# Kernel optimization log

Measured on AMD Instinct MI355X. Metric: run time of the kernel, lower is better.

## Reference

```python
import jax, jax.numpy as jnp
import numpy as np

# model dims
V, D, C, H, NL, E, EH = 32000, 256, 2, 8, 2, 8, 1024
B, S = 16, 512
DH = D // H
N = B * S


def _pos_encoding(length, d):
    pos = jnp.arange(length)[:, None].astype(jnp.float32)
    div = jnp.exp(jnp.arange(0, d, 2).astype(jnp.float32) * (-np.log(10000.0) / d))
    pe = jnp.zeros((length, d), dtype=jnp.float32)
    pe = pe.at[:, 0::2].set(jnp.sin(pos * div))
    pe = pe.at[:, 1::2].set(jnp.cos(pos * div))
    return pe


def _ln(x, g, b, eps=1e-5):
    mu = x.mean(-1, keepdims=True)
    var = ((x - mu) ** 2).mean(-1, keepdims=True)
    return (x - mu) / jnp.sqrt(var + eps) * g + b


def setup_inputs():
    key = jax.random.key(0)
    ks = jax.random.split(key, 12)
    n = lambda k, shape, s=0.02: (jax.random.normal(k, shape) * s).astype(jnp.float32)
    return dict(
        x=jax.random.randint(ks[0], (B, S), 0, V),
        emb=n(ks[1], (V, D), 0.1),
        in_proj_w=n(ks[2], (NL, 3 * D, D)),
        in_proj_b=jnp.zeros((NL, 3 * D), jnp.float32),
        out_proj_w=n(ks[3], (NL, D, D)),
        out_proj_b=jnp.zeros((NL, D), jnp.float32),
        ln1_g=jnp.ones((NL, D), jnp.float32), ln1_b=jnp.zeros((NL, D), jnp.float32),
        ln2_g=jnp.ones((NL, D), jnp.float32), ln2_b=jnp.zeros((NL, D), jnp.float32),
        gate_w=n(ks[4], (NL, E, D)), gate_b=jnp.zeros((NL, E), jnp.float32),
        w1=n(ks[5], (NL, E, EH, D)), b1=jnp.zeros((NL, E, EH), jnp.float32),
        w2=n(ks[6], (NL, E, D, EH)), b2=jnp.zeros((NL, E, D), jnp.float32),
        fc1_w=n(ks[7], (128, D), 0.1), fc1_b=jnp.zeros((128,), jnp.float32),
        fc2_w=n(ks[8], (C, 128), 0.1), fc2_b=jnp.zeros((C,), jnp.float32),
    )


def reference(x, emb, in_proj_w, in_proj_b, out_proj_w, out_proj_b,
              ln1_g, ln1_b, ln2_g, ln2_b, gate_w, gate_b,
              w1, b1, w2, b2, fc1_w, fc1_b, fc2_w, fc2_b):
    h = emb[x] * np.sqrt(float(D))                       # [B,S,D]
    h = h + _pos_encoding(S, D)[None]
    pad = h.sum(-1) == 0                                 # key padding mask [B,S]
    for l in range(NL):
        # --- multi-head self-attention ---
        qkv = h @ in_proj_w[l].T + in_proj_b[l]          # [B,S,3D]
        q, k, v = jnp.split(qkv, 3, axis=-1)
        q = q.reshape(B, S, H, DH).transpose(0, 2, 1, 3)
        k = k.reshape(B, S, H, DH).transpose(0, 2, 1, 3)
        v = v.reshape(B, S, H, DH).transpose(0, 2, 1, 3)
        sc = jnp.einsum('bhqd,bhkd->bhqk', q, k) / np.sqrt(float(DH))
        sc = jnp.where(pad[:, None, None, :], -1e9, sc)
        a = jax.nn.softmax(sc, axis=-1)
        ctx = jnp.einsum('bhqk,bhkd->bhqd', a, v).transpose(0, 2, 1, 3).reshape(B, S, D)
        attn_out = ctx @ out_proj_w[l].T + out_proj_b[l]
        h = _ln(h + attn_out, ln1_g[l], ln1_b[l])
        # --- top-1 MoE ---
        xf = h.reshape(N, D)
        gwt = jax.nn.softmax(xf @ gate_w[l].T + gate_b[l], axis=-1)  # [N,E]
        top_idx = jnp.argmax(gwt, axis=-1)                # [N]
        top_w = jnp.max(gwt, axis=-1)                     # [N]
        eh = jax.nn.relu(jnp.einsum('nd,ehd->enh', xf, w1[l]) + b1[l][:, None, :])
        ey = jnp.einsum('enh,edh->end', eh, w2[l]) + b2[l][:, None, :]  # [E,N,D]
        sel = ey[top_idx, jnp.arange(N)]                  # gather routed expert output [N,D]
        moe = (top_w[:, None] * sel).reshape(B, S, D)
        h = _ln(h + moe, ln2_g[l], ln2_b[l])
    m = (~pad)[..., None].astype(h.dtype)                 # [B,S,1]
    pooled = (h * m).sum(1) / jnp.clip(m.sum(1), 1.0)     # masked mean pool [B,D]
    z = jax.nn.relu(pooled @ fc1_w.T + fc1_b)
    return z @ fc2_w.T + fc2_b                            # [B,C]
```

## Files before the change

kernel.cpp:

```cpp
#include <hip/hip_runtime.h>
#include <math.h>

#define D_MODEL 256
#define NTOK    8192
#define SEQ     512
#define NB      16
#define NH      8
#define DHEAD   32
#define NE      8
#define EHID    1024
#define CSTRIDE 32

typedef __attribute__((ext_vector_type(8))) short short8;
typedef __attribute__((ext_vector_type(4))) float floatx4;
typedef unsigned short ushort_t;

__device__ __forceinline__ ushort_t bf16r(float f) {
    unsigned int u = __float_as_uint(f);
    u += 0x7fffu + ((u >> 16) & 1u);
    return (ushort_t)(u >> 16);
}
__device__ __forceinline__ float bf2f(ushort_t b) {
    return __uint_as_float(((unsigned)b) << 16);
}

#define GLD16(gsrc, ldst) \
    __builtin_amdgcn_global_load_lds( \
        (const __attribute__((address_space(1))) void*)(gsrc), \
        (__attribute__((address_space(3))) void*)(ldst), 16, 0, 0)

__global__ __launch_bounds__(256) void wconv_all(
    const float* __restrict__ in_proj_w, const float* __restrict__ out_proj_w,
    const float* __restrict__ w1, const float* __restrict__ w2,
    ushort_t* __restrict__ wball)
{
    const int g = blockIdx.x * 256 + threadIdx.x;
    const float* src; ushort_t* dst; int lo;
    if (g < 98304)        { src = in_proj_w;  dst = wball;           lo = g; }
    else if (g < 131072)  { src = out_proj_w; dst = wball + 393216;  lo = g - 98304; }
    else if (g < 1179648) { src = w1;         dst = wball + 524288;  lo = g - 131072; }
    else                  { src = w2;         dst = wball + 4718592; lo = g - 1179648; }
    float4 v = *(const float4*)(src + (size_t)lo * 4);
    ushort_t o[4] = { bf16r(v.x), bf16r(v.y), bf16r(v.z), bf16r(v.w) };
    *(uint2*)(dst + (size_t)lo * 4) = *(uint2*)o;
}

__global__ __launch_bounds__(256) void embed_kernel(
    const int* __restrict__ x, const float* __restrict__ emb,
    float* __restrict__ h, ushort_t* __restrict__ hb, int* __restrict__ pad)
{
    __shared__ float wred[4];
    const int n = blockIdx.x;
    const int d = threadIdx.x;
    const int wave = d >> 6;
    const int s = n & (SEQ - 1);
    const int tok = x[n];
    float v = emb[tok * D_MODEL + d] * 16.0f;
    const int j = d >> 1;
    const float c = -9.210340371976184f / 256.0f;
    const float div = expf((float)(2 * j) * c);
    const float ang = (float)s * div;
    v += (d & 1) ? cosf(ang) : sinf(ang);
    h[n * D_MODEL + d] = v;
    hb[n * D_MODEL + d] = bf16r(v);
    float sm = v;
    for (int o = 1; o < 64; o <<= 1) sm += __shfl_xor(sm, o);
    if ((d & 63) == 0) wred[wave] = sm;
    __syncthreads();
    if (d == 0) pad[n] = ((wred[0] + wred[1] + wred[2] + wred[3]) == 0.0f) ? 1 : 0;
}

#define GF_RELU    1
#define GF_OUTBF16 2
#define GF_GATHER  4
#define GF_SCATTER 8

__global__ __launch_bounds__(256) void gemm_gl64(
    const ushort_t* __restrict__ A, const ushort_t* __restrict__ Bw,
    const float* __restrict__ bias, void* __restrict__ Cout,
    int M, int N, int K,
    const int* __restrict__ counts,
    const int* __restrict__ perm, const float* __restrict__ topw,
    int flags)
{
    __shared__ ushort_t As[64 * 64];
    __shared__ ushort_t Bs[64 * 64];
    const int e = blockIdx.z;
    int cnt, off = 0;
    if (counts) {
        cnt = counts[e * CSTRIDE];
        if ((int)blockIdx.y * 64 >= cnt) return;
        for (int i = 0; i < e; i++) off += counts[i * CSTRIDE];
    } else { cnt = M; }
    const ushort_t* Bp = Bw + (size_t)e * N * K;
    const float* bp = bias + (size_t)e * N;
    const int m0 = blockIdx.y * 64, n0 = blockIdx.x * 64;
    const int tid = threadIdx.x;
    const int lane = tid & 63, wave = tid >> 6;
    const int r8 = lane >> 3;
    const int p  = lane & 7;
    const int kswz = ((p ^ r8) << 3);
    const int row0 = wave * 16;
    size_t asrc[2], bsrc[2];
#pragma unroll
    for (int c = 0; c < 2; c++) {
        const int gr = m0 + row0 + c * 8 + r8;
        const int grc = (gr < cnt) ? gr : m0;
        asrc[c] = (flags & GF_GATHER) ? (size_t)perm[off + grc] : (size_t)(off + grc);
        bsrc[c] = (size_t)(n0 + row0 + c * 8 + r8);
    }
    const int quad = lane >> 4, fr = lane & 15;
    const int wm = (wave & 1) * 32, wn = (wave >> 1) * 32;
    floatx4 acc[2][2];
#pragma unroll
    for (int i = 0; i < 2; i++)
#pragma unroll
        for (int jj = 0; jj < 2; jj++) acc[i][jj] = (floatx4){0.f, 0.f, 0.f, 0.f};

    for (int k0 = 0; k0 < K; k0 += 64) {
        __syncthreads();
#pragma unroll
        for (int c = 0; c < 2; c++) {
            GLD16(A + asrc[c] * K + k0 + kswz, &As[(row0 + c * 8) * 64]);
            GLD16(Bp + bsrc[c] * K + k0 + kswz, &Bs[(row0 + c * 8) * 64]);
        }
        __syncthreads();
#pragma unroll
        for (int ks = 0; ks < 2; ks++) {
            const int sw = (((ks * 4 + quad) ^ (fr & 7)) << 3);
            short8 fa0 = *(const short8*)&As[(wm + fr) * 64 + sw];
            short8 fa1 = *(const short8*)&As[(wm + 16 + fr) * 64 + sw];
            short8 fb0 = *(const short8*)&Bs[(wn + fr) * 64 + sw];
            short8 fb1 = *(const short8*)&Bs[(wn + 16 + fr) * 64 + sw];
            acc[0][0] = __builtin_amdgcn_mfma_f32_16x16x32_bf16(fa0, fb0, acc[0][0], 0, 0, 0);
            acc[0][1] = __builtin_amdgcn_mfma_f32_16x16x32_bf16(fa0, fb1, acc[0][1], 0, 0, 0);
            acc[1][0] = __builtin_amdgcn_mfma_f32_16x16x32_bf16(fa1, fb0, acc[1][0], 0, 0, 0);
            acc[1][1] = __builtin_amdgcn_mfma_f32_16x16x32_bf16(fa1, fb1, acc[1][1], 0, 0, 0);
        }
    }
    const int crow0 = quad * 4;
    const int ccol = fr;
#pragma unroll
    for (int m = 0; m < 2; m++) {
#pragma unroll
        for (int n = 0; n < 2; n++) {
            const int gcol = n0 + wn + n * 16 + ccol;
            const float bsv = bp[gcol];
#pragma unroll
            for (int r = 0; r < 4; r++) {
                const int grow = m0 + wm + m * 16 + crow0 + r;
                if (grow >= cnt) continue;
                float v = acc[m][n][r] + bsv;
                if (flags & GF_RELU) v = fmaxf(v, 0.f);
                if (flags & GF_SCATTER) {
                    const int tok = perm[off + grow];
                    ((float*)Cout)[(size_t)tok * N + gcol] = v * topw[tok];
                } else if (flags & GF_OUTBF16) {
                    ((ushort_t*)Cout)[(size_t)(off + grow) * N + gcol] = bf16r(v);
                } else {
                    ((float*)Cout)[(size_t)(off + grow) * N + gcol] = v;
                }
            }
        }
    }
}

__global__ __launch_bounds__(256) void attn_kernel(
    const ushort_t* __restrict__ qkvb, const int* __restrict__ pad,
    ushort_t* __restrict__ ctxb)
{
    __shared__ ushort_t Kt[64 * 40];
    __shared__ ushort_t Vt[32 * 72];
    __shared__ ushort_t Ps[64 * 72];
    __shared__ float padf[512];
    const int tid = threadIdx.x;
    const int lane = tid & 63;
    const int wave = tid >> 6;
    const int quad = lane >> 4;
    const int l16  = lane & 15;
    const int bid = blockIdx.x;
    const int qt = bid & 7;
    const int hh = (bid >> 3) & 7;
    const int b = bid >> 6;
    const int q0 = wave * 16;

    padf[tid]       = (float)pad[b * SEQ + tid];
    padf[tid + 256] = (float)pad[b * SEQ + 256 + tid];

    short8 qfrag = *(const short8*)(qkvb +
        (size_t)(b * SEQ + qt * 64 + q0 + l16) * 768 + hh * 32 + quad * 8);

    const int skey = tid >> 2;
    const int schunk = (tid & 3) * 8;

    floatx4 o0 = {0.f,0.f,0.f,0.f}, o1 = {0.f,0.f,0.f,0.f};
    float lsum[4] = {0.f, 0.f, 0.f, 0.f};
    const float scale = 0.17677669529663687f;

    for (int t = 0; t < 8; t++) {
        const int kbase = b * SEQ + t * 64;
        __syncthreads();
        uint4 kv = *(const uint4*)(qkvb + (size_t)(kbase + skey) * 768 + 256 + hh * 32 + schunk);
        *(uint4*)&Kt[skey * 40 + schunk] = kv;
        uint4 vv = *(const uint4*)(qkvb + (size_t)(kbase + skey) * 768 + 512 + hh * 32 + schunk);
        ushort_t vs[8]; *(uint4*)vs = vv;
#pragma unroll
        for (int j = 0; j < 8; j++) {
            const int d = schunk + j;
            Vt[d * 72 + (skey ^ ((d >> 3) << 3))] = vs[j];
        }
        __syncthreads();
        floatx4 sfr[4];
#pragma unroll
        for (int fn = 0; fn < 4; fn++) {
            short8 kf = *(const short8*)&Kt[(fn * 16 + l16) * 40 + quad * 8];
            sfr[fn] = __builtin_amdgcn_mfma_f32_16x16x32_bf16(
                qfrag, kf, (floatx4){0.f,0.f,0.f,0.f}, 0, 0, 0);
        }
#pragma unroll
        for (int fn = 0; fn < 4; fn++) {
            const int keyl = fn * 16 + l16;
            const float pv = padf[t * 64 + keyl];
#pragma unroll
            for (int r = 0; r < 4; r++) {
                float p = (pv != 0.f) ? 0.f : __expf(sfr[fn][r] * scale);
                ushort_t pb = bf16r(p);
                lsum[r] += bf2f(pb);
                Ps[(q0 + quad * 4 + r) * 72 + keyl] = pb;
            }
        }
#pragma unroll
        for (int kc = 0; kc < 2; kc++) {
            short8 pf = *(const short8*)&Ps[(q0 + l16) * 72 + kc * 32 + quad * 8];
            {
                const int d = l16;
                short8 vf = *(const short8*)&Vt[d * 72 + ((kc * 32 + quad * 8) ^ ((d >> 3) << 3))];
                o0 = __builtin_amdgcn_mfma_f32_16x16x32_bf16(pf, vf, o0, 0, 0, 0);
            }
            {
                const int d = 16 + l16;
                short8 vf = *(const short8*)&Vt[d * 72 + ((kc * 32 + quad * 8) ^ ((d >> 3) << 3))];
                o1 = __builtin_amdgcn_mfma_f32_16x16x32_bf16(pf, vf, o1, 0, 0, 0);
            }
        }
    }
#pragma unroll
    for (int r = 0; r < 4; r++) {
        float v = lsum[r];
        v += __shfl_xor(v, 1); v += __shfl_xor(v, 2);
        v += __shfl_xor(v, 4); v += __shfl_xor(v, 8);
        lsum[r] = 1.f / v;
    }
    const int nq = b * SEQ + qt * 64 + q0 + quad * 4;
#pragma unroll
    for (int r = 0; r < 4; r++) {
        ushort_t* outp = ctxb + (size_t)(nq + r) * 256 + hh * 32;
        outp[l16]      = bf16r(o0[r] * lsum[r]);
        outp[16 + l16] = bf16r(o1[r] * lsum[r]);
    }
}

template<bool GATE>
__global__ __launch_bounds__(256) void add_ln_t(
    float* __restrict__ h, const float* __restrict__ add,
    const float* __restrict__ g, const float* __restrict__ b,
    ushort_t* __restrict__ hb,
    const float* __restrict__ gw, const float* __restrict__ gb,
    int* __restrict__ top_idx, float* __restrict__ top_w)
{
    __shared__ float wred[8];
    __shared__ float ered[NE][4];
    const int n = blockIdx.x;
    const int d = threadIdx.x;
    const int wave = d >> 6;
    const float v = h[n * D_MODEL + d] + add[n * D_MODEL + d];
    float s = v;
    for (int o = 1; o < 64; o <<= 1) s += __shfl_xor(s, o);
    if ((d & 63) == 0) wred[wave] = s;
    __syncthreads();
    const float mu = (wred[0] + wred[1] + wred[2] + wred[3]) * (1.0f / 256.0f);
    const float c = v - mu;
    float cs = c * c;
    for (int o = 1; o < 64; o <<= 1) cs += __shfl_xor(cs, o);
    if ((d & 63) == 0) wred[4 + wave] = cs;
    __syncthreads();
    const float var = (wred[4] + wred[5] + wred[6] + wred[7]) * (1.0f / 256.0f);
    const float o = c * rsqrtf(var + 1e-5f) * g[d] + b[d];
    h[n * D_MODEL + d] = o;
    hb[n * D_MODEL + d] = bf16r(o);
    if (GATE) {
#pragma unroll
        for (int e = 0; e < NE; e++) {
            float pe = o * gw[e * D_MODEL + d];
            for (int of = 1; of < 64; of <<= 1) pe += __shfl_xor(pe, of);
            if ((d & 63) == 0) ered[e][wave] = pe;
        }
        __syncthreads();
        if (d == 0) {
            float best = -1e30f; int bi = 0;
            float lg[NE];
#pragma unroll
            for (int e = 0; e < NE; e++) {
                lg[e] = ered[e][0] + ered[e][1] + ered[e][2] + ered[e][3] + gb[e];
                if (lg[e] > best) { best = lg[e]; bi = e; }
            }
            float ssum = 0.0f;
#pragma unroll
            for (int e = 0; e < NE; e++) ssum += __expf(lg[e] - best);
            top_idx[n] = bi;
            top_w[n] = 1.0f / ssum;
        }
    }
}

__global__ __launch_bounds__(256) void bucket_kernel(
    const int* __restrict__ top_idx, int* __restrict__ pos,
    int* __restrict__ counts)
{
    __shared__ int hist[NE];
    __shared__ int base[NE];
    __shared__ int lpos[256];
    const int n = blockIdx.x * 256 + threadIdx.x;
    if (threadIdx.x < NE) hist[threadIdx.x] = 0;
    __syncthreads();
    const int e = top_idx[n];
    lpos[threadIdx.x] = atomicAdd(&hist[e], 1);
    __syncthreads();
    if (threadIdx.x < NE)
        base[threadIdx.x] = atomicAdd(&counts[threadIdx.x * CSTRIDE], hist[threadIdx.x]);
    __syncthreads();
    pos[n] = base[e] + lpos[threadIdx.x];
}

__global__ __launch_bounds__(256) void scatter_perm(
    const int* __restrict__ top_idx, const int* __restrict__ pos,
    const int* __restrict__ counts, int* __restrict__ perm)
{
    __shared__ int offs_s[NE];
    if (threadIdx.x < NE) {
        int a = 0;
        for (int i = 0; i < (int)threadIdx.x; i++) a += counts[i * CSTRIDE];
        offs_s[threadIdx.x] = a;
    }
    __syncthreads();
    const int n = blockIdx.x * 256 + threadIdx.x;
    if (n < NTOK) perm[offs_s[top_idx[n]] + pos[n]] = n;
}

__global__ __launch_bounds__(256) void pool1(
    const float* __restrict__ h, const int* __restrict__ pad,
    float* __restrict__ pooled, float* __restrict__ cntb)
{
    const int b = blockIdx.x, c = blockIdx.y, d = threadIdx.x;
    float s = 0.0f; int cnt = 0;
    for (int i = 0; i < 32; i++) {
        const int idx = b * SEQ + c * 32 + i;
        if (!pad[idx]) { s += h[(size_t)idx * D_MODEL + d]; cnt++; }
    }
    atomicAdd(&pooled[b * D_MODEL + d], s);
    if (d == 0) atomicAdd(&cntb[b], (float)cnt);
}

__global__ __launch_bounds__(128) void cls_kernel(
    const float* __restrict__ pooled, const float* __restrict__ cntb,
    const float* __restrict__ fc1w, const float* __restrict__ fc1b,
    const float* __restrict__ fc2w, const float* __restrict__ fc2b,
    float* __restrict__ out)
{
    __shared__ float zs[128];
    const int b = blockIdx.x;
    const int j = threadIdx.x;
    const float invc = 1.0f / fmaxf(cntb[b], 1.0f);
    float s = 0.0f;
    for (int d = 0; d < D_MODEL; d++) s += pooled[b * D_MODEL + d] * fc1w[j * D_MODEL + d];
    zs[j] = fmaxf(s * invc + fc1b[j], 0.0f);
    __syncthreads();
    if (j < 2) {
        float o = fc2b[j];
        for (int i = 0; i < 128; i++) o += zs[i] * fc2w[j * 128 + i];
        out[b * 2 + j] = o;
    }
}

extern "C" void kernel_launch(void* const* d_in, const int* in_sizes, int n_in,
                              void* d_out, int out_size, void* d_ws, size_t ws_size,
                              hipStream_t stream)
{
    const int*   x          = (const int*)d_in[0];
    const float* emb        = (const float*)d_in[1];
    const float* in_proj_w  = (const float*)d_in[2];
    const float* in_proj_b  = (const float*)d_in[3];
    const float* out_proj_w = (const float*)d_in[4];
    const float* out_proj_b = (const float*)d_in[5];
    const float* ln1_g      = (const float*)d_in[6];
    const float* ln1_b      = (const float*)d_in[7];
    const float* ln2_g      = (const float*)d_in[8];
    const float* ln2_b      = (const float*)d_in[9];
    const float* gate_w     = (const float*)d_in[10];
    const float* gate_b     = (const float*)d_in[11];
    const float* w1         = (const float*)d_in[12];
    const float* b1         = (const float*)d_in[13];
    const float* w2         = (const float*)d_in[14];
    const float* b2         = (const float*)d_in[15];
    const float* fc1_w      = (const float*)d_in[16];
    const float* fc1_b      = (const float*)d_in[17];
    const float* fc2_w      = (const float*)d_in[18];
    const float* fc2_b      = (const float*)d_in[19];
    float* out = (float*)d_out;

    float* ws = (float*)d_ws;
    float*    h      = ws;
    float*    tmp    = ws + 2097152;
    ushort_t* qkvb   = (ushort_t*)(ws + 4194304);
    ushort_t* ctxb   = (ushort_t*)(ws + 7340032);
    ushort_t* ehb    = (ushort_t*)(ws + 4194304);
    ushort_t* hb     = (ushort_t*)(ws + 8388608);
    float*    top_w  = ws + 9437184;
    float*    pooled = ws + 9445376;
    float*    cntb   = ws + 9449472;
    int*      counts = (int*)(ws + 9449488);
    int* ipart   = (int*)(ws + 9450000);
    int* pad     = ipart;
    int* top_idx = ipart + 8192;
    int* pos     = ipart + 16384;
    int* perm    = ipart + 24576;
    ushort_t* wball = (ushort_t*)(ws + 9482768);

    wconv_all<<<8704, 256, 0, stream>>>(in_proj_w, out_proj_w, w1, w2, wball);
    embed_kernel<<<NTOK, 256, 0, stream>>>(x, emb, h, hb, pad);
    hipMemsetAsync(pooled, 0, (4096 + 16 + 2 * NE * CSTRIDE) * sizeof(float), stream);

    for (int l = 0; l < 2; l++) {
        const ushort_t* inb_l  = wball + (size_t)l * 196608;
        const ushort_t* outb_l = wball + 393216 + (size_t)l * 65536;
        const ushort_t* w1b_l  = wball + 524288 + (size_t)l * 2097152;
        const ushort_t* w2b_l  = wball + 4718592 + (size_t)l * 2097152;
        int* counts_l = counts + l * NE * CSTRIDE;

        gemm_gl64<<<dim3(768 / 64, NTOK / 64, 1), 256, 0, stream>>>(
            hb, inb_l, in_proj_b + l * 768, qkvb, NTOK, 768, 256,
            nullptr, nullptr, nullptr, GF_OUTBF16);
        attn_kernel<<<NB * NH * (SEQ / 64), 256, 0, stream>>>(qkvb, pad, ctxb);
        gemm_gl64<<<dim3(256 / 64, NTOK / 64, 1), 256, 0, stream>>>(
            ctxb, outb_l, out_proj_b + l * 256, tmp, NTOK, 256, 256,
            nullptr, nullptr, nullptr, 0);
        add_ln_t<true><<<NTOK, 256, 0, stream>>>(
            h, tmp, ln1_g + l * 256, ln1_b + l * 256, hb,
            gate_w + l * NE * 256, gate_b + l * NE, top_idx, top_w);
        bucket_kernel<<<NTOK / 256, 256, 0, stream>>>(top_idx, pos, counts_l);
        scatter_perm<<<NTOK / 256, 256, 0, stream>>>(top_idx, pos, counts_l, perm);
        gemm_gl64<<<dim3(EHID / 64, NTOK / 64, NE), 256, 0, stream>>>(
            hb, w1b_l, b1 + l * NE * EHID, ehb, 0, EHID, 256,
            counts_l, perm, nullptr, GF_GATHER | GF_RELU | GF_OUTBF16);
        gemm_gl64<<<dim3(D_MODEL / 64, NTOK / 64, NE), 256, 0, stream>>>(
            ehb, w2b_l, b2 + l * NE * 256, tmp, 0, D_MODEL, 1024,
            counts_l, perm, top_w, GF_SCATTER);
        add_ln_t<false><<<NTOK, 256, 0, stream>>>(
            h, tmp, ln2_g + l * 256, ln2_b + l * 256, hb,
            nullptr, nullptr, nullptr, nullptr);
    }

    pool1<<<dim3(NB, 16), 256, 0, stream>>>(h, pad, pooled, cntb);
    cls_kernel<<<NB, 128, 0, stream>>>(pooled, cntb, fc1_w, fc1_b, fc2_w, fc2_b, out);
}
```

Before: 443.1 us.

## Fuse out-proj and expert FC2 GEMMs with residual add, LayerNorm and gating

Replaces the out-projection GEMM plus separate add+LayerNorm+gate kernel with one kernel that computes 16-row tiles over the full 256-column width, then does residual, LayerNorm and top-1 gating in registers. The expert FC2 GEMM is likewise fused with the weighted scatter, residual add and second LayerNorm, which removes the fp32 tmp round trip and two launches per layer. In exchange the tiles are only 16 rows tall, so each block reloads the full weight slice. Variance now comes from a single-pass E[x^2]-mu^2 formula, which is slightly less numerically stable.

After: 397.9 us. -10.2%, faster.

```diff
diff --git a/kernel.cpp b/kernel.cpp
--- a/kernel.cpp
+++ b/kernel.cpp
@@ -19,9 +19,6 @@
     unsigned int u = __float_as_uint(f);
     u += 0x7fffu + ((u >> 16) & 1u);
     return (ushort_t)(u >> 16);
-}
-__device__ __forceinline__ float bf2f(ushort_t b) {
-    return __uint_as_float(((unsigned)b) << 16);
 }
 
 #define GLD16(gsrc, ldst) \
@@ -165,6 +162,245 @@
     }
 }
 
+__global__ __launch_bounds__(256) void oproj_ln(
+    const ushort_t* __restrict__ Actx, const ushort_t* __restrict__ Wb,
+    const float* __restrict__ bias, float* __restrict__ h,
+    ushort_t* __restrict__ hb,
+    const float* __restrict__ g, const float* __restrict__ b,
+    const float* __restrict__ gw, const float* __restrict__ gb,
+    int* __restrict__ top_idx, float* __restrict__ top_w)
+{
+    __shared__ ushort_t As[16 * 64];
+    __shared__ ushort_t Bs[256 * 64];
+    __shared__ float lsum[16][4], lsq[16][4];
+    __shared__ float gred[16][NE][4];
+    const int m0 = blockIdx.x * 16;
+    const int tid = threadIdx.x;
+    const int lane = tid & 63, wave = tid >> 6;
+    const int r8 = lane >> 3, p = lane & 7;
+    const int kswz = ((p ^ r8) << 3);
+    const int quad = lane >> 4, fr = lane & 15;
+    const int wn = wave * 64;
+    floatx4 acc[4];
+#pragma unroll
+    for (int n = 0; n < 4; n++) acc[n] = (floatx4){0.f, 0.f, 0.f, 0.f};
+
+    for (int k0 = 0; k0 < 256; k0 += 64) {
+        __syncthreads();
+        if (wave < 2)
+            GLD16(Actx + (size_t)(m0 + wave * 8 + r8) * 256 + k0 + kswz,
+                  &As[(wave * 8) * 64]);
+#pragma unroll
+        for (int c = 0; c < 8; c++)
+            GLD16(Wb + (size_t)(wn + c * 8 + r8) * 256 + k0 + kswz,
+                  &Bs[(wn + c * 8) * 64]);
+        __syncthreads();
+#pragma unroll
+        for (int ks = 0; ks < 2; ks++) {
+            const int sw = (((ks * 4 + quad) ^ (fr & 7)) << 3);
+            short8 fa = *(const short8*)&As[fr * 64 + sw];
+#pragma unroll
+            for (int n = 0; n < 4; n++) {
+                short8 fb = *(const short8*)&Bs[(wn + n * 16 + fr) * 64 + sw];
+                acc[n] = __builtin_amdgcn_mfma_f32_16x16x32_bf16(fa, fb, acc[n], 0, 0, 0);
+            }
+        }
+    }
+    const int rbase = quad * 4;
+    float val[4][4];
+#pragma unroll
+    for (int n = 0; n < 4; n++) {
+        const int col = wn + n * 16 + fr;
+        const float bsv = bias[col];
+#pragma unroll
+        for (int r = 0; r < 4; r++)
+            val[r][n] = acc[n][r] + bsv + h[(size_t)(m0 + rbase + r) * 256 + col];
+    }
+    float s[4], sq[4];
+#pragma unroll
+    for (int r = 0; r < 4; r++) {
+        s[r]  = val[r][0] + val[r][1] + val[r][2] + val[r][3];
+        sq[r] = val[r][0] * val[r][0] + val[r][1] * val[r][1]
+              + val[r][2] * val[r][2] + val[r][3] * val[r][3];
+    }
+#pragma unroll
+    for (int ox = 1; ox < 16; ox <<= 1)
+#pragma unroll
+        for (int r = 0; r < 4; r++) {
+            s[r] += __shfl_xor(s[r], ox);
+            sq[r] += __shfl_xor(sq[r], ox);
+        }
+    if (fr == 0)
+#pragma unroll
+        for (int r = 0; r < 4; r++) { lsum[rbase + r][wave] = s[r]; lsq[rbase + r][wave] = sq[r]; }
+    __syncthreads();
+    float mu[4], rstd[4];
+#pragma unroll
+    for (int r = 0; r < 4; r++) {
+        const int row = rbase + r;
+        const float m = (lsum[row][0] + lsum[row][1] + lsum[row][2] + lsum[row][3]) * (1.f / 256.f);
+        float v2 = (lsq[row][0] + lsq[row][1] + lsq[row][2] + lsq[row][3]) * (1.f / 256.f) - m * m;
+        mu[r] = m;
+        rstd[r] = rsqrtf(fmaxf(v2, 0.f) + 1e-5f);
+    }
+    float o4[4][4];
+#pragma unroll
+    for (int n = 0; n < 4; n++) {
+        const int col = wn + n * 16 + fr;
+        const float gc = g[col], bc = b[col];
+#pragma unroll
+        for (int r = 0; r < 4; r++) {
+            const float o = (val[r][n] - mu[r]) * rstd[r] * gc + bc;
+            o4[r][n] = o;
+            const size_t idx = (size_t)(m0 + rbase + r) * 256 + col;
+            h[idx] = o;
+            hb[idx] = bf16r(o);
+        }
+    }
+#pragma unroll
+    for (int e = 0; e < NE; e++) {
+        float ge[4] = {0.f, 0.f, 0.f, 0.f};
+#pragma unroll
+        for (int n = 0; n < 4; n++) {
+            const float gwv = gw[e * 256 + wn + n * 16 + fr];
+#pragma unroll
+            for (int r = 0; r < 4; r++) ge[r] += o4[r][n] * gwv;
+        }
+#pragma unroll
+        for (int ox = 1; ox < 16; ox <<= 1)
+#pragma unroll
+            for (int r = 0; r < 4; r++) ge[r] += __shfl_xor(ge[r], ox);
+        if (fr == 0)
+#pragma unroll
+            for (int r = 0; r < 4; r++) gred[rbase + r][e][wave] = ge[r];
+    }
+    __syncthreads();
+    if (tid < 16) {
+        const int row = tid;
+        float lg[NE];
+        float best = -1e30f; int bi = 0;
+#pragma unroll
+        for (int e = 0; e < NE; e++) {
+            lg[e] = gred[row][e][0] + gred[row][e][1] + gred[row][e][2] + gred[row][e][3] + gb[e];
+            if (lg[e] > best) { best = lg[e]; bi = e; }
+        }
+        float ssum = 0.f;
+#pragma unroll
+        for (int e = 0; e < NE; e++) ssum += __expf(lg[e] - best);
+        top_idx[m0 + row] = bi;
+        top_w[m0 + row] = 1.f / ssum;
+    }
+}
+
+__global__ __launch_bounds__(256) void fc2_ln(
+    const ushort_t* __restrict__ ehb, const ushort_t* __restrict__ Wb,
+    const float* __restrict__ b2, const int* __restrict__ counts,
+    const int* __restrict__ perm, const float* __restrict__ topw,
+    float* __restrict__ h, ushort_t* __restrict__ hb,
+    const float* __restrict__ g, const float* __restrict__ b)
+{
+    __shared__ ushort_t As[16 * 64];
+    __shared__ ushort_t Bs[256 * 64];
+    __shared__ float lsum[16][4], lsq[16][4];
+    const int e = blockIdx.y;
+    const int cnt = counts[e * CSTRIDE];
+    const int m0 = blockIdx.x * 16;
+    if (m0 >= cnt) return;
+    int off = 0;
+    for (int i = 0; i < e; i++) off += counts[i * CSTRIDE];
+    const ushort_t* Wp = Wb + (size_t)e * 256 * 1024;
+    const float* bp = b2 + e * 256;
+    const int tid = threadIdx.x;
+    const int lane = tid & 63, wave = tid >> 6;
+    const int r8 = lane >> 3, p = lane & 7;
+    const int kswz = ((p ^ r8) << 3);
+    const int quad = lane >> 4, fr = lane & 15;
+    const int wn = wave * 64;
+    size_t arow = 0;
+    if (wave < 2) {
+        const int gr = m0 + wave * 8 + r8;
+        arow = (size_t)(off + ((gr < cnt) ? gr : m0));
+    }
+    floatx4 acc[4];
+#pragma unroll
+    for (int n = 0; n < 4; n++) acc[n] = (floatx4){0.f, 0.f, 0.f, 0.f};
+
+    for (int k0 = 0; k0 < 1024; k0 += 64) {
+        __syncthreads();
+        if (wave < 2)
+            GLD16(ehb + arow * 1024 + k0 + kswz, &As[(wave * 8) * 64]);
+#pragma unroll
+        for (int c = 0; c < 8; c++)
+            GLD16(Wp + (size_t)(wn + c * 8 + r8) * 1024 + k0 + kswz,
+                  &Bs[(wn + c * 8) * 64]);
+        __syncthreads();
+#pragma unroll
+        for (int ks = 0; ks < 2; ks++) {
+            const int sw = (((ks * 4 + quad) ^ (fr & 7)) << 3);
+            short8 fa = *(const short8*)&As[fr * 64 + sw];
+#pragma unroll
+            for (int n = 0; n < 4; n++) {
+                short8 fb = *(const short8*)&Bs[(wn + n * 16 + fr) * 64 + sw];
+                acc[n] = __builtin_amdgcn_mfma_f32_16x16x32_bf16(fa, fb, acc[n], 0, 0, 0);
+            }
+        }
+    }
+    const int rbase = quad * 4;
+    int tokr[4]; bool vld[4]; float twr[4];
+#pragma unroll
+    for (int r = 0; r < 4; r++) {
+        const int grow = m0 + rbase + r;
+        vld[r] = grow < cnt;
+        tokr[r] = perm[off + (vld[r] ? grow : 0)];
+        twr[r] = topw[tokr[r]];
+    }
+    float val[4][4];
+#pragma unroll
+    for (int n = 0; n < 4; n++) {
+        const int col = wn + n * 16 + fr;
+        const float bsv = bp[col];
+#pragma unroll
+        for (int r = 0; r < 4; r++)
+            val[r][n] = vld[r]
+                ? (acc[n][r] + bsv) * twr[r] + h[(size_t)tokr[r] * 256 + col]
+                : 0.f;
+    }
+    float s[4], sq[4];
+#pragma unroll
+    for (int r = 0; r < 4; r++) {
+        s[r]  = val[r][0] + val[r][1] + val[r][2] + val[r][3];
+        sq[r] = val[r][0] * val[r][0] + val[r][1] * val[r][1]
+              + val[r][2] * val[r][2] + val[r][3] * val[r][3];
+    }
+#pragma unroll
+    for (int ox = 1; ox < 16; ox <<= 1)
+#pragma unroll
+        for (int r = 0; r < 4; r++) {
+            s[r] += __shfl_xor(s[r], ox);
+            sq[r] += __shfl_xor(sq[r], ox);
+        }
+    if (fr == 0)
+#pragma unroll
+        for (int r = 0; r < 4; r++) { lsum[rbase + r][wave] = s[r]; lsq[rbase + r][wave] = sq[r]; }
+    __syncthreads();
+#pragma unroll
+    for (int r = 0; r < 4; r++) {
+        if (!vld[r]) continue;
+        const int row = rbase + r;
+        const float m = (lsum[row][0] + lsum[row][1] + lsum[row][2] + lsum[row][3]) * (1.f / 256.f);
+        float v2 = (lsq[row][0] + lsq[row][1] + lsq[row][2] + lsq[row][3]) * (1.f / 256.f) - m * m;
+        const float rstd = rsqrtf(fmaxf(v2, 0.f) + 1e-5f);
+#pragma unroll
+        for (int n = 0; n < 4; n++) {
+            const int col = wn + n * 16 + fr;
+            const float o = (val[r][n] - m) * rstd * g[col] + b[col];
+            const size_t idx = (size_t)tokr[r] * 256 + col;
+            h[idx] = o;
+            hb[idx] = bf16r(o);
+        }
+    }
+}
+
 __global__ __launch_bounds__(256) void attn_kernel(
     const ushort_t* __restrict__ qkvb, const int* __restrict__ pad,
     ushort_t* __restrict__ ctxb)
@@ -194,7 +430,7 @@
     const int schunk = (tid & 3) * 8;
 
     floatx4 o0 = {0.f,0.f,0.f,0.f}, o1 = {0.f,0.f,0.f,0.f};
-    float lsum[4] = {0.f, 0.f, 0.f, 0.f};
+    float lsumr[4] = {0.f, 0.f, 0.f, 0.f};
     const float scale = 0.17677669529663687f;
 
     for (int t = 0; t < 8; t++) {
@@ -223,9 +459,9 @@
             const float pv = padf[t * 64 + keyl];
 #pragma unroll
             for (int r = 0; r < 4; r++) {
-                float p = (pv != 0.f) ? 0.f : __expf(sfr[fn][r] * scale);
-                ushort_t pb = bf16r(p);
-                lsum[r] += bf2f(pb);
+                float pr = (pv != 0.f) ? 0.f : __expf(sfr[fn][r] * scale);
+                ushort_t pb = bf16r(pr);
+                lsumr[r] += __uint_as_float(((unsigned)pb) << 16);
                 Ps[(q0 + quad * 4 + r) * 72 + keyl] = pb;
             }
         }
@@ -246,70 +482,17 @@
     }
 #pragma unroll
     for (int r = 0; r < 4; r++) {
-        float v = lsum[r];
+        float v = lsumr[r];
         v += __shfl_xor(v, 1); v += __shfl_xor(v, 2);
         v += __shfl_xor(v, 4); v += __shfl_xor(v, 8);
-        lsum[r] = 1.f / v;
+        lsumr[r] = 1.f / v;
     }
     const int nq = b * SEQ + qt * 64 + q0 + quad * 4;
 #pragma unroll
     for (int r = 0; r < 4; r++) {
         ushort_t* outp = ctxb + (size_t)(nq + r) * 256 + hh * 32;
-        outp[l16]      = bf16r(o0[r] * lsum[r]);
-        outp[16 + l16] = bf16r(o1[r] * lsum[r]);
-    }
-}
-
-template<bool GATE>
-__global__ __launch_bounds__(256) void add_ln_t(
-    float* __restrict__ h, const float* __restrict__ add,
-    const float* __restrict__ g, const float* __restrict__ b,
-    ushort_t* __restrict__ hb,
-    const float* __restrict__ gw, const float* __restrict__ gb,
-    int* __restrict__ top_idx, float* __restrict__ top_w)
-{
-    __shared__ float wred[8];
-    __shared__ float ered[NE][4];
-    const int n = blockIdx.x;
-    const int d = threadIdx.x;
-    const int wave = d >> 6;
-    const float v = h[n * D_MODEL + d] + add[n * D_MODEL + d];
-    float s = v;
-    for (int o = 1; o < 64; o <<= 1) s += __shfl_xor(s, o);
-    if ((d & 63) == 0) wred[wave] = s;
-    __syncthreads();
-    const float mu = (wred[0] + wred[1] + wred[2] + wred[3]) * (1.0f / 256.0f);
-    const float c = v - mu;
-    float cs = c * c;
-    for (int o = 1; o < 64; o <<= 1) cs += __shfl_xor(cs, o);
-    if ((d & 63) == 0) wred[4 + wave] = cs;
-    __syncthreads();
-    const float var = (wred[4] + wred[5] + wred[6] + wred[7]) * (1.0f / 256.0f);
-    const float o = c * rsqrtf(var + 1e-5f) * g[d] + b[d];
-    h[n * D_MODEL + d] = o;
-    hb[n * D_MODEL + d] = bf16r(o);
-    if (GATE) {
-#pragma unroll
-        for (int e = 0; e < NE; e++) {
-            float pe = o * gw[e * D_MODEL + d];
-            for (int of = 1; of < 64; of <<= 1) pe += __shfl_xor(pe, of);
-            if ((d & 63) == 0) ered[e][wave] = pe;
-        }
-        __syncthreads();
-        if (d == 0) {
-            float best = -1e30f; int bi = 0;
-            float lg[NE];
-#pragma unroll
-            for (int e = 0; e < NE; e++) {
-                lg[e] = ered[e][0] + ered[e][1] + ered[e][2] + ered[e][3] + gb[e];
-                if (lg[e] > best) { best = lg[e]; bi = e; }
-            }
-            float ssum = 0.0f;
-#pragma unroll
-            for (int e = 0; e < NE; e++) ssum += __expf(lg[e] - best);
-            top_idx[n] = bi;
-            top_w[n] = 1.0f / ssum;
-        }
+        outp[l16]      = bf16r(o0[r] * lsumr[r]);
+        outp[16 + l16] = bf16r(o1[r] * lsumr[r]);
     }
 }
 
@@ -410,7 +593,6 @@
 
     float* ws = (float*)d_ws;
     float*    h      = ws;
-    float*    tmp    = ws + 2097152;
     ushort_t* qkvb   = (ushort_t*)(ws + 4194304);
     ushort_t* ctxb   = (ushort_t*)(ws + 7340032);
     ushort_t* ehb    = (ushort_t*)(ws + 4194304);
@@ -441,23 +623,18 @@
             hb, inb_l, in_proj_b + l * 768, qkvb, NTOK, 768, 256,
             nullptr, nullptr, nullptr, GF_OUTBF16);
         attn_kernel<<<NB * NH * (SEQ / 64), 256, 0, stream>>>(qkvb, pad, ctxb);
-        gemm_gl64<<<dim3(256 / 64, NTOK / 64, 1), 256, 0, stream>>>(
-            ctxb, outb_l, out_proj_b + l * 256, tmp, NTOK, 256, 256,
-            nullptr, nullptr, nullptr, 0);
-        add_ln_t<true><<<NTOK, 256, 0, stream>>>(
-            h, tmp, ln1_g + l * 256, ln1_b + l * 256, hb,
+        oproj_ln<<<NTOK / 16, 256, 0, stream>>>(
+            ctxb, outb_l, out_proj_b + l * 256, h, hb,
+            ln1_g + l * 256, ln1_b + l * 256,
             gate_w + l * NE * 256, gate_b + l * NE, top_idx, top_w);
         bucket_kernel<<<NTOK / 256, 256, 0, stream>>>(top_idx, pos, counts_l);
         scatter_perm<<<NTOK / 256, 256, 0, stream>>>(top_idx, pos, counts_l, perm);
         gemm_gl64<<<dim3(EHID / 64, NTOK / 64, NE), 256, 0, stream>>>(
             hb, w1b_l, b1 + l * NE * EHID, ehb, 0, EHID, 256,
             counts_l, perm, nullptr, GF_GATHER | GF_RELU | GF_OUTBF16);
-        gemm_gl64<<<dim3(D_MODEL / 64, NTOK / 64, NE), 256, 0, stream>>>(
-            ehb, w2b_l, b2 + l * NE * 256, tmp, 0, D_MODEL, 1024,
-            counts_l, perm, top_w, GF_SCATTER);
-        add_ln_t<false><<<NTOK, 256, 0, stream>>>(
-            h, tmp, ln2_g + l * 256, ln2_b + l * 256, hb,
-            nullptr, nullptr, nullptr, nullptr);
+        fc2_ln<<<dim3(NTOK / 16, NE), 256, 0, stream>>>(
+            ehb, w2b_l, b2 + l * NE * 256, counts_l, perm, top_w,
+            h, hb, ln2_g + l * 256, ln2_b + l * 256);
     }
 
     pool1<<<dim3(NB, 16), 256, 0, stream>>>(h, pad, pooled, cntb);
```
